# Kernel tuning notes

Hardware: AMD Instinct MI355X
Metric: run time of the kernel (lower is better)

Reference implementation:

```python
import jax, jax.numpy as jnp
import numpy as np

N = 100000
IN = 128
HID = 128
E = 1000000
EP = 100000


def setup_inputs() -> dict:
    key = jax.random.key(0)
    ks = jax.random.split(key, 20)
    inp = {
        "x": jax.random.normal(ks[0], (N, IN), dtype=jnp.float32),
        "edge_src1": jax.random.randint(ks[1], (E,), 0, N),
        "edge_dst1": jax.random.randint(ks[2], (E,), 0, N),
        "edge_src2": jax.random.randint(ks[3], (E,), 0, N),
        "edge_dst2": jax.random.randint(ks[4], (E,), 0, N),
        "pos_src": jax.random.randint(ks[5], (EP,), 0, N),
        "pos_dst": jax.random.randint(ks[6], (EP,), 0, N),
        "neg_src": jax.random.randint(ks[7], (EP,), 0, N),
        "neg_dst": jax.random.randint(ks[8], (EP,), 0, N),
        # SAGEConv layer 1 (in->hid): fc_self (no bias), fc_neigh, shared bias
        "W_self1": jax.random.normal(ks[9], (IN, HID), dtype=jnp.float32) * (1.0 / np.sqrt(IN)),
        "W_neigh1": jax.random.normal(ks[10], (IN, HID), dtype=jnp.float32) * (1.0 / np.sqrt(IN)),
        "b1": jnp.zeros((HID,), dtype=jnp.float32),
        # SAGEConv layer 2 (hid->hid)
        "W_self2": jax.random.normal(ks[11], (HID, HID), dtype=jnp.float32) * (1.0 / np.sqrt(HID)),
        "W_neigh2": jax.random.normal(ks[12], (HID, HID), dtype=jnp.float32) * (1.0 / np.sqrt(HID)),
        "b2": jnp.zeros((HID,), dtype=jnp.float32),
        # predictor: Linear(hid,hid) -> ReLU -> Linear(hid,1)
        "Wp1": jax.random.normal(ks[13], (HID, HID), dtype=jnp.float32) * (1.0 / np.sqrt(HID)),
        "bp1": jnp.zeros((HID,), dtype=jnp.float32),
        "Wp2": jax.random.normal(ks[14], (HID, 1), dtype=jnp.float32) * (1.0 / np.sqrt(HID)),
        "bp2": jnp.zeros((1,), dtype=jnp.float32),
    }
    return inp


def _sage_conv(h, src, dst, W_self, W_neigh, b):
    # mean aggregation over incoming edges: gather h[src], scatter-add to dst, divide by degree
    agg = jax.ops.segment_sum(h[src], dst, num_segments=N)          # [N, d]
    deg = jax.ops.segment_sum(jnp.ones((src.shape[0],), h.dtype), dst, num_segments=N)
    mean = agg / jnp.maximum(deg, 1.0)[:, None]
    return h @ W_self + mean @ W_neigh + b


def _predictor(z, Wp1, bp1, Wp2, bp2):
    return jax.nn.relu(z @ Wp1 + bp1) @ Wp2 + bp2                   # [Ep, 1]


def reference(x, edge_src1, edge_dst1, edge_src2, edge_dst2,
              pos_src, pos_dst, neg_src, neg_dst,
              W_self1, W_neigh1, b1, W_self2, W_neigh2, b2,
              Wp1, bp1, Wp2, bp2):
    h = jax.nn.relu(_sage_conv(x, edge_src1, edge_dst1, W_self1, W_neigh1, b1))
    h = _sage_conv(h, edge_src2, edge_dst2, W_self2, W_neigh2, b2)  # [N, HID]
    h_pos = _predictor(h[pos_src] * h[pos_dst], Wp1, bp1, Wp2, bp2)
    h_neg = _predictor(h[neg_src] * h[neg_dst], Wp1, bp1, Wp2, bp2)
    return (h_pos, h_neg)
```

## Files before the change

kernel.cpp:

```cpp
#include <hip/hip_runtime.h>

typedef unsigned short ushort_t;
typedef __attribute__((ext_vector_type(8))) short short8;
typedef __attribute__((ext_vector_type(4))) float f32x4;

constexpr int NN = 100000;
constexpr int D  = 128;
constexpr int NE = 1000000;
constexpr int NP = 100000;

constexpr int BK_SHIFT = 9;
constexpr int NBK_L = (NN + 511) >> BK_SHIFT;
constexpr int NBK   = 2 * NBK_L;
constexpr int ACHUNK = 4096;
constexpr int ABLOCKS = (2 * NE + ACHUNK - 1) / ACHUNK;

__device__ __forceinline__ float bf2f(ushort_t u) {
    union { unsigned int i; float f; } v; v.i = ((unsigned int)u) << 16; return v.f;
}
__device__ __forceinline__ ushort_t f2bf(float x) {
    union { float f; unsigned int i; } v; v.f = x;
    unsigned int r = v.i + 0x7fffu + ((v.i >> 16) & 1u);
    return (ushort_t)(r >> 16);
}
__device__ __forceinline__ void split2(float x, ushort_t& h, ushort_t& l) {
    h = f2bf(x);
    l = f2bf(x - bf2f(h));
}

__global__ void __launch_bounds__(256) prep_kernel(
    const float* __restrict__ x,
    const float* __restrict__ Ws1, const float* __restrict__ Wn1,
    const float* __restrict__ Ws2, const float* __restrict__ Wn2,
    const float* __restrict__ Wp1,
    ushort_t* __restrict__ xh, ushort_t* __restrict__ xl,
    ushort_t* __restrict__ w1h, ushort_t* __restrict__ w1l,
    ushort_t* __restrict__ w2h, ushort_t* __restrict__ w2l,
    ushort_t* __restrict__ wph, ushort_t* __restrict__ wpl)
{
    int b = blockIdx.x;
    if (b < 12500) {
        int tid = b * 256 + threadIdx.x;
        float4 v = *reinterpret_cast<const float4*>(x + (size_t)tid * 4);
        ushort4 h4, l4;
        split2(v.x, h4.x, l4.x); split2(v.y, h4.y, l4.y);
        split2(v.z, h4.z, l4.z); split2(v.w, h4.w, l4.w);
        *reinterpret_cast<ushort4*>(xh + (size_t)tid * 4) = h4;
        *reinterpret_cast<ushort4*>(xl + (size_t)tid * 4) = l4;
    } else if (b < 12756) {
        int layer2 = (b >= 12628);
        int tid = (b - (layer2 ? 12628 : 12500)) * 256 + threadIdx.x;
        int k = tid >> 7, n = tid & 127;
        const float* Ws = layer2 ? Ws2 : Ws1;
        const float* Wn = layer2 ? Wn2 : Wn1;
        ushort_t* Wth = layer2 ? w2h : w1h;
        ushort_t* Wtl = layer2 ? w2l : w1l;
        float v = (k < 128) ? Ws[k * 128 + n] : Wn[(k - 128) * 128 + n];
        ushort_t h, l; split2(v, h, l);
        Wth[n * 256 + k] = h; Wtl[n * 256 + k] = l;
    } else {
        int tid = (b - 12756) * 256 + threadIdx.x;
        int k = tid >> 7, n = tid & 127;
        float v = Wp1[k * 128 + n];
        ushort_t h, l; split2(v, h, l);
        wph[n * 128 + k] = h; wpl[n * 128 + k] = l;
    }
}

__global__ void __launch_bounds__(256) bucket_count_kernel(
    const int* __restrict__ ed1, const int* __restrict__ ed2,
    int* __restrict__ btot)
{
    __shared__ int hist[NBK];
    int t = threadIdx.x;
    for (int i = t; i < NBK; i += 256) hist[i] = 0;
    __syncthreads();
    int base = blockIdx.x * ACHUNK;
    for (int it = 0; it < ACHUNK / 256; ++it) {
        int e = base + it * 256 + t;
        if (e < 2 * NE) {
            int layer2 = (e >= NE);
            int d = layer2 ? ed2[e - NE] : ed1[e];
            atomicAdd(&hist[(layer2 ? NBK_L : 0) + (d >> BK_SHIFT)], 1);
        }
    }
    __syncthreads();
    for (int i = t; i < NBK; i += 256)
        if (hist[i]) atomicAdd(&btot[i], hist[i]);
}

__global__ void __launch_bounds__(512) bucket_scan_kernel(
    const int* __restrict__ btot, int* __restrict__ bbase, int* __restrict__ bcur)
{
    __shared__ int s[512];
    int t = threadIdx.x;
    int v = (t < NBK) ? btot[t] : 0;
    s[t] = v;
    __syncthreads();
    for (int off = 1; off < 512; off <<= 1) {
        int u = (t >= off) ? s[t - off] : 0;
        __syncthreads();
        s[t] += u;
        __syncthreads();
    }
    if (t < NBK) {
        int ex = s[t] - v;
        bbase[t] = ex;
        bcur[t] = ex;
        if (t == NBK - 1) bbase[NBK] = s[t];
    }
}

__global__ void __launch_bounds__(256) bucket_scatter_kernel(
    const int* __restrict__ es1, const int* __restrict__ ed1,
    const int* __restrict__ es2, const int* __restrict__ ed2,
    int* __restrict__ bcur, int2* __restrict__ pair)
{
    __shared__ int hist[NBK];
    __shared__ int rbase[NBK];
    __shared__ int cur[NBK];
    int t = threadIdx.x;
    for (int i = t; i < NBK; i += 256) hist[i] = 0;
    __syncthreads();
    int base = blockIdx.x * ACHUNK;
    for (int it = 0; it < ACHUNK / 256; ++it) {
        int e = base + it * 256 + t;
        if (e < 2 * NE) {
            int layer2 = (e >= NE);
            int d = layer2 ? ed2[e - NE] : ed1[e];
            atomicAdd(&hist[(layer2 ? NBK_L : 0) + (d >> BK_SHIFT)], 1);
        }
    }
    __syncthreads();
    for (int i = t; i < NBK; i += 256) {
        int h = hist[i];
        rbase[i] = h ? atomicAdd(&bcur[i], h) : 0;
        cur[i] = 0;
    }
    __syncthreads();
    for (int it = 0; it < ACHUNK / 256; ++it) {
        int e = base + it * 256 + t;
        if (e < 2 * NE) {
            int layer2 = (e >= NE);
            int s = layer2 ? es2[e - NE] : es1[e];
            int d = layer2 ? ed2[e - NE] : ed1[e];
            int bkt = (layer2 ? NBK_L : 0) + (d >> BK_SHIFT);
            int r = atomicAdd(&cur[bkt], 1);
            pair[(size_t)rbase[bkt] + r] = make_int2(s, d);
        }
    }
}

__global__ void __launch_bounds__(256) bucket_build_kernel(
    const int2* __restrict__ pair, const int* __restrict__ bbase,
    int* __restrict__ row_off, int* __restrict__ csr)
{
    __shared__ int cnt[512];
    __shared__ int sc[256];
    int b = blockIdx.x;
    int t = threadIdx.x;
    int layer2 = (b >= NBK_L);
    int n0 = (b - (layer2 ? NBK_L : 0)) << BK_SHIFT;
    int nodes = min(512, NN - n0);
    int gnode0 = n0 + (layer2 ? NN : 0);
    int e0 = bbase[b], e1 = bbase[b + 1];
    int m = e1 - e0;

    cnt[t] = 0; cnt[t + 256] = 0;
    __syncthreads();
    for (int j = t; j < m; j += 256)
        atomicAdd(&cnt[pair[(size_t)e0 + j].y - n0], 1);
    __syncthreads();

    int a0 = cnt[2 * t], a1 = cnt[2 * t + 1];
    sc[t] = a0 + a1;
    __syncthreads();
    for (int off = 1; off < 256; off <<= 1) {
        int u = (t >= off) ? sc[t - off] : 0;
        __syncthreads();
        sc[t] += u;
        __syncthreads();
    }
    int ex = sc[t] - (a0 + a1);
    cnt[2 * t] = ex;
    cnt[2 * t + 1] = ex + a0;
    __syncthreads();

    for (int i = t; i < nodes; i += 256)
        row_off[gnode0 + i] = e0 + cnt[i];
    if (b == NBK - 1 && t == 0) row_off[2 * NN] = 2 * NE;
    __syncthreads();

    for (int j = t; j < m; j += 256) {
        int2 p = pair[(size_t)e0 + j];
        int r = atomicAdd(&cnt[p.y - n0], 1);
        csr[(size_t)e0 + r] = p.x;
    }
}

__global__ void __launch_bounds__(256) gather_mean_kernel(
    const float* __restrict__ feat,
    const int* __restrict__ row_off,
    const int* __restrict__ csr,
    ushort_t* __restrict__ mh, ushort_t* __restrict__ ml)
{
    int tid = blockIdx.x * 256 + threadIdx.x;
    int g = tid >> 5;
    int lane = tid & 31;
    int c = lane << 2;
    int beg = row_off[g], end = row_off[g + 1];
    float ax0 = 0.f, ay0 = 0.f, az0 = 0.f, aw0 = 0.f;
    float ax1 = 0.f, ay1 = 0.f, az1 = 0.f, aw1 = 0.f;
    int j = beg;
    for (; j + 8 <= end; j += 8) {
        int s0 = csr[j + 0], s1 = csr[j + 1], s2 = csr[j + 2], s3 = csr[j + 3];
        int s4 = csr[j + 4], s5 = csr[j + 5], s6 = csr[j + 6], s7 = csr[j + 7];
        float4 v0 = *reinterpret_cast<const float4*>(feat + (size_t)s0 * D + c);
        float4 v1 = *reinterpret_cast<const float4*>(feat + (size_t)s1 * D + c);
        float4 v2 = *reinterpret_cast<const float4*>(feat + (size_t)s2 * D + c);
        float4 v3 = *reinterpret_cast<const float4*>(feat + (size_t)s3 * D + c);
        float4 v4 = *reinterpret_cast<const float4*>(feat + (size_t)s4 * D + c);
        float4 v5 = *reinterpret_cast<const float4*>(feat + (size_t)s5 * D + c);
        float4 v6 = *reinterpret_cast<const float4*>(feat + (size_t)s6 * D + c);
        float4 v7 = *reinterpret_cast<const float4*>(feat + (size_t)s7 * D + c);
        ax0 += v0.x + v1.x + v4.x + v5.x; ay0 += v0.y + v1.y + v4.y + v5.y;
        az0 += v0.z + v1.z + v4.z + v5.z; aw0 += v0.w + v1.w + v4.w + v5.w;
        ax1 += v2.x + v3.x + v6.x + v7.x; ay1 += v2.y + v3.y + v6.y + v7.y;
        az1 += v2.z + v3.z + v6.z + v7.z; aw1 += v2.w + v3.w + v6.w + v7.w;
    }
    for (; j < end; ++j) {
        int s = csr[j];
        float4 v = *reinterpret_cast<const float4*>(feat + (size_t)s * D + c);
        ax0 += v.x; ay0 += v.y; az0 += v.z; aw0 += v.w;
    }
    float rd = 1.0f / fmaxf((float)(end - beg), 1.0f);
    float mx = (ax0 + ax1) * rd, my = (ay0 + ay1) * rd;
    float mz = (az0 + az1) * rd, mw = (aw0 + aw1) * rd;
    ushort4 h4, l4;
    split2(mx, h4.x, l4.x); split2(my, h4.y, l4.y);
    split2(mz, h4.z, l4.z); split2(mw, h4.w, l4.w);
    *reinterpret_cast<ushort4*>(mh + (size_t)g * D + c) = h4;
    *reinterpret_cast<ushort4*>(ml + (size_t)g * D + c) = l4;
}

template<bool RELU, bool WSPLIT, bool WF32>
__global__ void __launch_bounds__(512) mfma_sage_gemm(
    const ushort_t* __restrict__ Ah_self, const ushort_t* __restrict__ Al_self,
    const ushort_t* __restrict__ Ah_nei,  const ushort_t* __restrict__ Al_nei,
    const ushort_t* __restrict__ Wth, const ushort_t* __restrict__ Wtl,
    const float* __restrict__ bias,
    ushort_t* __restrict__ out_h, ushort_t* __restrict__ out_l,
    float* __restrict__ out_f)
{
    __shared__ short Bh[128 * 64];
    __shared__ short Bl[128 * 64];

    int t = threadIdx.x;
    int l = t & 63, w = t >> 6;
    int lrow = l & 15, kg = l >> 4;
    int row0 = blockIdx.x * 128;
    int arow = row0 + w * 16 + lrow;
    int arow_c = min(arow, NN - 1);

    f32x4 acc[8];
    for (int i = 0; i < 8; ++i) acc[i] = (f32x4)(0.f);

    for (int half = 0; half < 2; ++half) {
        const ushort_t* Ah = half ? Ah_nei : Ah_self;
        const ushort_t* Al = half ? Al_nei : Al_self;
        for (int kc2 = 0; kc2 < 2; ++kc2) {
            int kcat = half * 128 + kc2 * 64;
            __syncthreads();
            for (int i = 0; i < 2; ++i) {
                int s = t + i * 512;
                int n = s >> 3;
                int k8 = (s & 7) * 8;
                short8 vh = *reinterpret_cast<const short8*>(Wth + n * 256 + kcat + k8);
                short8 vl = *reinterpret_cast<const short8*>(Wtl + n * 256 + kcat + k8);
                int db = n * 128 + ((k8 * 2) ^ ((n & 7) << 4));
                *reinterpret_cast<short8*>((char*)Bh + db) = vh;
                *reinterpret_cast<short8*>((char*)Bl + db) = vl;
            }
            __syncthreads();

            for (int ks = 0; ks < 2; ++ks) {
                int ka = kc2 * 64 + ks * 32 + kg * 8;
                short8 ah = *reinterpret_cast<const short8*>(Ah + (size_t)arow_c * D + ka);
                short8 al = *reinterpret_cast<const short8*>(Al + (size_t)arow_c * D + ka);
                int kb2 = (ks * 32 + kg * 8) * 2;
                for (int ct = 0; ct < 8; ++ct) {
                    int n = ct * 16 + lrow;
                    int db = n * 128 + (kb2 ^ ((n & 7) << 4));
                    short8 bh = *reinterpret_cast<const short8*>((char*)Bh + db);
                    short8 bl = *reinterpret_cast<const short8*>((char*)Bl + db);
                    acc[ct] = __builtin_amdgcn_mfma_f32_16x16x32_bf16(ah, bh, acc[ct], 0, 0, 0);
                    acc[ct] = __builtin_amdgcn_mfma_f32_16x16x32_bf16(ah, bl, acc[ct], 0, 0, 0);
                    acc[ct] = __builtin_amdgcn_mfma_f32_16x16x32_bf16(al, bh, acc[ct], 0, 0, 0);
                }
            }
        }
    }

    for (int ct = 0; ct < 8; ++ct) {
        int n = ct * 16 + lrow;
        float bv = bias[n];
        for (int j = 0; j < 4; ++j) {
            int r = row0 + w * 16 + kg * 4 + j;
            if (r >= NN) continue;
            float y = acc[ct][j] + bv;
            if (RELU) y = fmaxf(y, 0.f);
            if (WF32) out_f[(size_t)r * D + n] = y;
            if (WSPLIT) {
                ushort_t hh, ll; split2(y, hh, ll);
                out_h[(size_t)r * D + n] = hh;
                out_l[(size_t)r * D + n] = ll;
            }
        }
    }
}

__global__ void __launch_bounds__(512) mfma_predictor(
    const float* __restrict__ H,
    const int* __restrict__ ps, const int* __restrict__ pd,
    const int* __restrict__ ns, const int* __restrict__ nd,
    const ushort_t* __restrict__ Wth, const ushort_t* __restrict__ Wtl,
    const float* __restrict__ bp1,
    const float* __restrict__ Wp2, const float* __restrict__ bp2,
    float* __restrict__ out)
{
    __shared__ short Zh[64 * 128];
    __shared__ short Zl[64 * 128];
    __shared__ short Bh[128 * 64];
    __shared__ short Bl[128 * 64];
    __shared__ float red[2][64];

    int t = threadIdx.x;
    int l = t & 63, w = t >> 6;
    int rt = w >> 1, ch = w & 1;
    int lrow = l & 15, kg = l >> 4;
    int row0 = blockIdx.x * 64;

    for (int i = 0; i < 4; ++i) {
        int idx = t + i * 512;
        int r = idx >> 5;
        int c4 = (idx & 31) << 2;
        int p = row0 + r;
        int s  = (p < NP) ? ps[p] : ns[p - NP];
        int d2 = (p < NP) ? pd[p] : nd[p - NP];
        float4 a = *reinterpret_cast<const float4*>(H + (size_t)s * D + c4);
        float4 b = *reinterpret_cast<const float4*>(H + (size_t)d2 * D + c4);
        float z0 = a.x * b.x, z1 = a.y * b.y, z2 = a.z * b.z, z3 = a.w * b.w;
        ushort4 h4, l4;
        split2(z0, h4.x, l4.x); split2(z1, h4.y, l4.y);
        split2(z2, h4.z, l4.z); split2(z3, h4.w, l4.w);
        int db = r * 256 + ((c4 * 2) ^ ((r & 7) << 4));
        *reinterpret_cast<ushort4*>((char*)Zh + db) = h4;
        *reinterpret_cast<ushort4*>((char*)Zl + db) = l4;
    }

    f32x4 acc[4];
    for (int i = 0; i < 4; ++i) acc[i] = (f32x4)(0.f);

    for (int kc = 0; kc < 2; ++kc) {
        __syncthreads();
        for (int i = 0; i < 2; ++i) {
            int s = t + i * 512;
            int n = s >> 3;
            int k8 = (s & 7) * 8;
            short8 vh = *reinterpret_cast<const short8*>(Wth + n * 128 + kc * 64 + k8);
            short8 vl = *reinterpret_cast<const short8*>(Wtl + n * 128 + kc * 64 + k8);
            int db = n * 128 + ((k8 * 2) ^ ((n & 7) << 4));
            *reinterpret_cast<short8*>((char*)Bh + db) = vh;
            *reinterpret_cast<short8*>((char*)Bl + db) = vl;
        }
        __syncthreads();

        for (int ks = 0; ks < 2; ++ks) {
            int zrow = rt * 16 + lrow;
            int kz2 = (kc * 64 + ks * 32 + kg * 8) * 2;
            int za = zrow * 256 + (kz2 ^ ((zrow & 7) << 4));
            short8 ah = *reinterpret_cast<const short8*>((char*)Zh + za);
            short8 al = *reinterpret_cast<const short8*>((char*)Zl + za);
            int kb2 = (ks * 32 + kg * 8) * 2;
            for (int ct = 0; ct < 4; ++ct) {
                int n = ch * 64 + ct * 16 + lrow;
                int db = n * 128 + (kb2 ^ ((n & 7) << 4));
                short8 bh = *reinterpret_cast<const short8*>((char*)Bh + db);
                short8 bl = *reinterpret_cast<const short8*>((char*)Bl + db);
                acc[ct] = __builtin_amdgcn_mfma_f32_16x16x32_bf16(ah, bh, acc[ct], 0, 0, 0);
                acc[ct] = __builtin_amdgcn_mfma_f32_16x16x32_bf16(ah, bl, acc[ct], 0, 0, 0);
                acc[ct] = __builtin_amdgcn_mfma_f32_16x16x32_bf16(al, bh, acc[ct], 0, 0, 0);
            }
        }
    }

    float partial[4] = {0.f, 0.f, 0.f, 0.f};
    for (int ct = 0; ct < 4; ++ct) {
        int n = ch * 64 + ct * 16 + lrow;
        float bv = bp1[n];
        float w2 = Wp2[n];
        for (int j = 0; j < 4; ++j) {
            float y = acc[ct][j] + bv;
            partial[j] += fmaxf(y, 0.f) * w2;
        }
    }
    for (int j = 0; j < 4; ++j)
        for (int off = 8; off >= 1; off >>= 1)
            partial[j] += __shfl_xor(partial[j], off);
    if (lrow == 0)
        for (int j = 0; j < 4; ++j)
            red[ch][rt * 16 + kg * 4 + j] = partial[j];
    __syncthreads();
    if (t < 64)
        out[row0 + t] = red[0][t] + red[1][t] + bp2[0];
}

extern "C" void kernel_launch(void* const* d_in, const int* in_sizes, int n_in,
                              void* d_out, int out_size, void* d_ws, size_t ws_size,
                              hipStream_t stream) {
    const float* x   = (const float*)d_in[0];
    const int*   es1 = (const int*)d_in[1];
    const int*   ed1 = (const int*)d_in[2];
    const int*   es2 = (const int*)d_in[3];
    const int*   ed2 = (const int*)d_in[4];
    const int*   ps  = (const int*)d_in[5];
    const int*   pd  = (const int*)d_in[6];
    const int*   ns  = (const int*)d_in[7];
    const int*   nd  = (const int*)d_in[8];
    const float* Ws1 = (const float*)d_in[9];
    const float* Wn1 = (const float*)d_in[10];
    const float* b1  = (const float*)d_in[11];
    const float* Ws2 = (const float*)d_in[12];
    const float* Wn2 = (const float*)d_in[13];
    const float* b2  = (const float*)d_in[14];
    const float* Wp1 = (const float*)d_in[15];
    const float* bp1 = (const float*)d_in[16];
    const float* Wp2 = (const float*)d_in[17];
    const float* bp2 = (const float*)d_in[18];
    float* out = (float*)d_out;

    char* ws = (char*)d_ws;
    size_t halfb = (size_t)NN * D * sizeof(ushort_t);
    ushort_t* x_h    = (ushort_t*)(ws);
    ushort_t* x_l    = (ushort_t*)(ws + halfb);
    ushort_t* mean_h = (ushort_t*)(ws + 2 * halfb);
    ushort_t* mean_l = (ushort_t*)(ws + 3 * halfb);
    float*    hf     = (float*)(ws + 4 * halfb);
    int2*     pair   = (int2*)hf;
    char* wsp = ws + 4 * halfb + (size_t)NN * D * sizeof(float);
    ushort_t* w1t_h  = (ushort_t*)wsp;
    ushort_t* w1t_l  = w1t_h + 256 * 128;
    ushort_t* w2t_h  = w1t_l + 256 * 128;
    ushort_t* w2t_l  = w2t_h + 256 * 128;
    ushort_t* wpt_h  = w2t_l + 256 * 128;
    ushort_t* wpt_l  = wpt_h + 128 * 128;
    int* row_off = (int*)(wpt_l + 128 * 128 + 64);
    int* csr     = row_off + 2 * NN + 2;
    int* btot    = csr + 2 * NE;
    int* bbase   = btot + NBK;
    int* bcur    = bbase + NBK + 1;

    dim3 blk(256), blk512(512);
    int gatherBlocks = NN * 32 / 256;
    int gemmBlocks   = (NN + 127) / 128;
    int predBlocks   = 2 * NP / 64;

    hipMemsetAsync(btot, 0, NBK * sizeof(int), stream);
    prep_kernel<<<12820, blk, 0, stream>>>(
        x, Ws1, Wn1, Ws2, Wn2, Wp1,
        x_h, x_l, w1t_h, w1t_l, w2t_h, w2t_l, wpt_h, wpt_l);
    bucket_count_kernel<<<ABLOCKS, blk, 0, stream>>>(ed1, ed2, btot);
    bucket_scan_kernel<<<1, 512, 0, stream>>>(btot, bbase, bcur);
    bucket_scatter_kernel<<<ABLOCKS, blk, 0, stream>>>(es1, ed1, es2, ed2, bcur, pair);
    bucket_build_kernel<<<NBK, blk, 0, stream>>>(pair, bbase, row_off, csr);

    gather_mean_kernel<<<gatherBlocks, blk, 0, stream>>>(x, row_off, csr, mean_h, mean_l);
    mfma_sage_gemm<true, true, true><<<gemmBlocks, blk512, 0, stream>>>(
        x_h, x_l, mean_h, mean_l, w1t_h, w1t_l, b1, x_h, x_l, hf);

    gather_mean_kernel<<<gatherBlocks, blk, 0, stream>>>(hf, row_off + NN, csr, mean_h, mean_l);
    mfma_sage_gemm<false, false, true><<<gemmBlocks, blk512, 0, stream>>>(
        x_h, x_l, mean_h, mean_l, w2t_h, w2t_l, b2, nullptr, nullptr, hf);

    mfma_predictor<<<predBlocks, blk512, 0, stream>>>(
        hf, ps, pd, ns, nd, wpt_h, wpt_l, bp1, Wp2, bp2, out);
}
```

Baseline: 366.4 us.

## Fuse neighbor mean gather into SAGE GEMM with LDS-staged split-bf16 tiles

```diff
diff --git a/kernel.cpp b/kernel.cpp
--- a/kernel.cpp
+++ b/kernel.cpp
@@ -15,6 +15,10 @@
 constexpr int ACHUNK = 4096;
 constexpr int ABLOCKS = (2 * NE + ACHUNK - 1) / ACHUNK;
 
+constexpr int PB_W   = 256;
+constexpr int PB_WP  = PB_W + 64;
+constexpr int PB_CNT = PB_WP + ABLOCKS;
+
 __device__ __forceinline__ float bf2f(ushort_t u) {
     union { unsigned int i; float f; } v; v.i = ((unsigned int)u) << 16; return v.f;
 }
@@ -29,27 +33,21 @@
 }
 
 __global__ void __launch_bounds__(256) prep_kernel(
-    const float* __restrict__ x,
     const float* __restrict__ Ws1, const float* __restrict__ Wn1,
     const float* __restrict__ Ws2, const float* __restrict__ Wn2,
     const float* __restrict__ Wp1,
-    ushort_t* __restrict__ xh, ushort_t* __restrict__ xl,
+    const int* __restrict__ ed1, const int* __restrict__ ed2,
     ushort_t* __restrict__ w1h, ushort_t* __restrict__ w1l,
     ushort_t* __restrict__ w2h, ushort_t* __restrict__ w2l,
-    ushort_t* __restrict__ wph, ushort_t* __restrict__ wpl)
-{
+    ushort_t* __restrict__ wph, ushort_t* __restrict__ wpl,
+    int* __restrict__ btot)
+{
+    __shared__ int hist[NBK];
     int b = blockIdx.x;
-    if (b < 12500) {
-        int tid = b * 256 + threadIdx.x;
-        float4 v = *reinterpret_cast<const float4*>(x + (size_t)tid * 4);
-        ushort4 h4, l4;
-        split2(v.x, h4.x, l4.x); split2(v.y, h4.y, l4.y);
-        split2(v.z, h4.z, l4.z); split2(v.w, h4.w, l4.w);
-        *reinterpret_cast<ushort4*>(xh + (size_t)tid * 4) = h4;
-        *reinterpret_cast<ushort4*>(xl + (size_t)tid * 4) = l4;
-    } else if (b < 12756) {
-        int layer2 = (b >= 12628);
-        int tid = (b - (layer2 ? 12628 : 12500)) * 256 + threadIdx.x;
+    int t = threadIdx.x;
+    if (b < PB_W) {
+        int layer2 = (b >= 128);
+        int tid = (b - (layer2 ? 128 : 0)) * 256 + t;
         int k = tid >> 7, n = tid & 127;
         const float* Ws = layer2 ? Ws2 : Ws1;
         const float* Wn = layer2 ? Wn2 : Wn1;
@@ -58,35 +56,28 @@
         float v = (k < 128) ? Ws[k * 128 + n] : Wn[(k - 128) * 128 + n];
         ushort_t h, l; split2(v, h, l);
         Wth[n * 256 + k] = h; Wtl[n * 256 + k] = l;
-    } else {
-        int tid = (b - 12756) * 256 + threadIdx.x;
+    } else if (b < PB_WP) {
+        int tid = (b - PB_W) * 256 + t;
         int k = tid >> 7, n = tid & 127;
         float v = Wp1[k * 128 + n];
         ushort_t h, l; split2(v, h, l);
         wph[n * 128 + k] = h; wpl[n * 128 + k] = l;
-    }
-}
-
-__global__ void __launch_bounds__(256) bucket_count_kernel(
-    const int* __restrict__ ed1, const int* __restrict__ ed2,
-    int* __restrict__ btot)
-{
-    __shared__ int hist[NBK];
-    int t = threadIdx.x;
-    for (int i = t; i < NBK; i += 256) hist[i] = 0;
-    __syncthreads();
-    int base = blockIdx.x * ACHUNK;
-    for (int it = 0; it < ACHUNK / 256; ++it) {
-        int e = base + it * 256 + t;
-        if (e < 2 * NE) {
-            int layer2 = (e >= NE);
-            int d = layer2 ? ed2[e - NE] : ed1[e];
-            atomicAdd(&hist[(layer2 ? NBK_L : 0) + (d >> BK_SHIFT)], 1);
-        }
-    }
-    __syncthreads();
-    for (int i = t; i < NBK; i += 256)
-        if (hist[i]) atomicAdd(&btot[i], hist[i]);
+    } else {
+        for (int i = t; i < NBK; i += 256) hist[i] = 0;
+        __syncthreads();
+        int base = (b - PB_WP) * ACHUNK;
+        for (int it = 0; it < ACHUNK / 256; ++it) {
+            int e = base + it * 256 + t;
+            if (e < 2 * NE) {
+                int layer2 = (e >= NE);
+                int d = layer2 ? ed2[e - NE] : ed1[e];
+                atomicAdd(&hist[(layer2 ? NBK_L : 0) + (d >> BK_SHIFT)], 1);
+            }
+        }
+        __syncthreads();
+        for (int i = t; i < NBK; i += 256)
+            if (hist[i]) atomicAdd(&btot[i], hist[i]);
+    }
 }
 
 __global__ void __launch_bounds__(512) bucket_scan_kernel(
@@ -198,81 +189,77 @@
     }
 }
 
-__global__ void __launch_bounds__(256) gather_mean_kernel(
+template<bool RELU>
+__global__ void __launch_bounds__(256) fused_conv_kernel(
     const float* __restrict__ feat,
     const int* __restrict__ row_off,
     const int* __restrict__ csr,
-    ushort_t* __restrict__ mh, ushort_t* __restrict__ ml)
-{
-    int tid = blockIdx.x * 256 + threadIdx.x;
-    int g = tid >> 5;
-    int lane = tid & 31;
-    int c = lane << 2;
-    int beg = row_off[g], end = row_off[g + 1];
-    float ax0 = 0.f, ay0 = 0.f, az0 = 0.f, aw0 = 0.f;
-    float ax1 = 0.f, ay1 = 0.f, az1 = 0.f, aw1 = 0.f;
-    int j = beg;
-    for (; j + 8 <= end; j += 8) {
-        int s0 = csr[j + 0], s1 = csr[j + 1], s2 = csr[j + 2], s3 = csr[j + 3];
-        int s4 = csr[j + 4], s5 = csr[j + 5], s6 = csr[j + 6], s7 = csr[j + 7];
-        float4 v0 = *reinterpret_cast<const float4*>(feat + (size_t)s0 * D + c);
-        float4 v1 = *reinterpret_cast<const float4*>(feat + (size_t)s1 * D + c);
-        float4 v2 = *reinterpret_cast<const float4*>(feat + (size_t)s2 * D + c);
-        float4 v3 = *reinterpret_cast<const float4*>(feat + (size_t)s3 * D + c);
-        float4 v4 = *reinterpret_cast<const float4*>(feat + (size_t)s4 * D + c);
-        float4 v5 = *reinterpret_cast<const float4*>(feat + (size_t)s5 * D + c);
-        float4 v6 = *reinterpret_cast<const float4*>(feat + (size_t)s6 * D + c);
-        float4 v7 = *reinterpret_cast<const float4*>(feat + (size_t)s7 * D + c);
-        ax0 += v0.x + v1.x + v4.x + v5.x; ay0 += v0.y + v1.y + v4.y + v5.y;
-        az0 += v0.z + v1.z + v4.z + v5.z; aw0 += v0.w + v1.w + v4.w + v5.w;
-        ax1 += v2.x + v3.x + v6.x + v7.x; ay1 += v2.y + v3.y + v6.y + v7.y;
-        az1 += v2.z + v3.z + v6.z + v7.z; aw1 += v2.w + v3.w + v6.w + v7.w;
-    }
-    for (; j < end; ++j) {
-        int s = csr[j];
-        float4 v = *reinterpret_cast<const float4*>(feat + (size_t)s * D + c);
-        ax0 += v.x; ay0 += v.y; az0 += v.z; aw0 += v.w;
-    }
-    float rd = 1.0f / fmaxf((float)(end - beg), 1.0f);
-    float mx = (ax0 + ax1) * rd, my = (ay0 + ay1) * rd;
-    float mz = (az0 + az1) * rd, mw = (aw0 + aw1) * rd;
-    ushort4 h4, l4;
-    split2(mx, h4.x, l4.x); split2(my, h4.y, l4.y);
-    split2(mz, h4.z, l4.z); split2(mw, h4.w, l4.w);
-    *reinterpret_cast<ushort4*>(mh + (size_t)g * D + c) = h4;
-    *reinterpret_cast<ushort4*>(ml + (size_t)g * D + c) = l4;
-}
-
-template<bool RELU, bool WSPLIT, bool WF32>
-__global__ void __launch_bounds__(512) mfma_sage_gemm(
-    const ushort_t* __restrict__ Ah_self, const ushort_t* __restrict__ Al_self,
-    const ushort_t* __restrict__ Ah_nei,  const ushort_t* __restrict__ Al_nei,
     const ushort_t* __restrict__ Wth, const ushort_t* __restrict__ Wtl,
     const float* __restrict__ bias,
-    ushort_t* __restrict__ out_h, ushort_t* __restrict__ out_l,
-    float* __restrict__ out_f)
-{
+    float* __restrict__ out)
+{
+    __shared__ short Mh[64 * 128];
+    __shared__ short Ml[64 * 128];
     __shared__ short Bh[128 * 64];
     __shared__ short Bl[128 * 64];
 
     int t = threadIdx.x;
+    int row0 = blockIdx.x * 64;
+
+    {
+        int gi = t >> 5, lane = t & 31, c = lane << 2;
+        for (int rr = gi; rr < 64; rr += 8) {
+            int node = min(row0 + rr, NN - 1);
+            int j = row_off[node], e = row_off[node + 1];
+            int deg = e - j;
+            float ax0 = 0.f, ay0 = 0.f, az0 = 0.f, aw0 = 0.f;
+            float ax1 = 0.f, ay1 = 0.f, az1 = 0.f, aw1 = 0.f;
+            for (; j + 8 <= e; j += 8) {
+                int s0 = csr[j], s1 = csr[j+1], s2 = csr[j+2], s3 = csr[j+3];
+                int s4 = csr[j+4], s5 = csr[j+5], s6 = csr[j+6], s7 = csr[j+7];
+                float4 v0 = *reinterpret_cast<const float4*>(feat + (size_t)s0 * D + c);
+                float4 v1 = *reinterpret_cast<const float4*>(feat + (size_t)s1 * D + c);
+                float4 v2 = *reinterpret_cast<const float4*>(feat + (size_t)s2 * D + c);
+                float4 v3 = *reinterpret_cast<const float4*>(feat + (size_t)s3 * D + c);
+                float4 v4 = *reinterpret_cast<const float4*>(feat + (size_t)s4 * D + c);
+                float4 v5 = *reinterpret_cast<const float4*>(feat + (size_t)s5 * D + c);
+                float4 v6 = *reinterpret_cast<const float4*>(feat + (size_t)s6 * D + c);
+                float4 v7 = *reinterpret_cast<const float4*>(feat + (size_t)s7 * D + c);
+                ax0 += v0.x + v1.x + v4.x + v5.x; ay0 += v0.y + v1.y + v4.y + v5.y;
+                az0 += v0.z + v1.z + v4.z + v5.z; aw0 += v0.w + v1.w + v4.w + v5.w;
+                ax1 += v2.x + v3.x + v6.x + v7.x; ay1 += v2.y + v3.y + v6.y + v7.y;
+                az1 += v2.z + v3.z + v6.z + v7.z; aw1 += v2.w + v3.w + v6.w + v7.w;
+            }
+            for (; j < e; ++j) {
+                int s = csr[j];
+                float4 v = *reinterpret_cast<const float4*>(feat + (size_t)s * D + c);
+                ax0 += v.x; ay0 += v.y; az0 += v.z; aw0 += v.w;
+            }
+            float rd = 1.0f / fmaxf((float)deg, 1.0f);
+            float mx = (ax0 + ax1) * rd, my = (ay0 + ay1) * rd;
+            float mz = (az0 + az1) * rd, mw = (aw0 + aw1) * rd;
+            ushort4 h4, l4;
+            split2(mx, h4.x, l4.x); split2(my, h4.y, l4.y);
+            split2(mz, h4.z, l4.z); split2(mw, h4.w, l4.w);
+            int db = rr * 256 + ((c * 2) ^ ((rr & 7) << 4));
+            *reinterpret_cast<ushort4*>((char*)Mh + db) = h4;
+            *reinterpret_cast<ushort4*>((char*)Ml + db) = l4;
+        }
+    }
+
     int l = t & 63, w = t >> 6;
     int lrow = l & 15, kg = l >> 4;
-    int row0 = blockIdx.x * 128;
-    int arow = row0 + w * 16 + lrow;
-    int arow_c = min(arow, NN - 1);
+    int arow_c = min(row0 + w * 16 + lrow, NN - 1);
 
     f32x4 acc[8];
     for (int i = 0; i < 8; ++i) acc[i] = (f32x4)(0.f);
 
     for (int half = 0; half < 2; ++half) {
-        const ushort_t* Ah = half ? Ah_nei : Ah_self;
-        const ushort_t* Al = half ? Al_nei : Al_self;
         for (int kc2 = 0; kc2 < 2; ++kc2) {
             int kcat = half * 128 + kc2 * 64;
             __syncthreads();
-            for (int i = 0; i < 2; ++i) {
-                int s = t + i * 512;
+            for (int i = 0; i < 4; ++i) {
+                int s = t + i * 256;
                 int n = s >> 3;
                 int k8 = (s & 7) * 8;
                 short8 vh = *reinterpret_cast<const short8*>(Wth + n * 256 + kcat + k8);
@@ -285,8 +272,26 @@
 
             for (int ks = 0; ks < 2; ++ks) {
                 int ka = kc2 * 64 + ks * 32 + kg * 8;
-                short8 ah = *reinterpret_cast<const short8*>(Ah + (size_t)arow_c * D + ka);
-                short8 al = *reinterpret_cast<const short8*>(Al + (size_t)arow_c * D + ka);
+                short8 ah, al;
+                if (half == 0) {
+                    const float* p = feat + (size_t)arow_c * D + ka;
+                    float4 v0 = *reinterpret_cast<const float4*>(p);
+                    float4 v1 = *reinterpret_cast<const float4*>(p + 4);
+                    ushort_t hh, ll;
+                    split2(v0.x, hh, ll); ah[0] = hh; al[0] = ll;
+                    split2(v0.y, hh, ll); ah[1] = hh; al[1] = ll;
+                    split2(v0.z, hh, ll); ah[2] = hh; al[2] = ll;
+                    split2(v0.w, hh, ll); ah[3] = hh; al[3] = ll;
+                    split2(v1.x, hh, ll); ah[4] = hh; al[4] = ll;
+                    split2(v1.y, hh, ll); ah[5] = hh; al[5] = ll;
+                    split2(v1.z, hh, ll); ah[6] = hh; al[6] = ll;
+                    split2(v1.w, hh, ll); ah[7] = hh; al[7] = ll;
+                } else {
+                    int row = w * 16 + lrow;
+                    int db = row * 256 + ((ka * 2) ^ ((row & 7) << 4));
+                    ah = *reinterpret_cast<const short8*>((char*)Mh + db);
+                    al = *reinterpret_cast<const short8*>((char*)Ml + db);
+                }
                 int kb2 = (ks * 32 + kg * 8) * 2;
                 for (int ct = 0; ct < 8; ++ct) {
                     int n = ct * 16 + lrow;
@@ -309,12 +314,7 @@
             if (r >= NN) continue;
             float y = acc[ct][j] + bv;
             if (RELU) y = fmaxf(y, 0.f);
-            if (WF32) out_f[(size_t)r * D + n] = y;
-            if (WSPLIT) {
-                ushort_t hh, ll; split2(y, hh, ll);
-                out_h[(size_t)r * D + n] = hh;
-                out_l[(size_t)r * D + n] = ll;
-            }
+            out[(size_t)r * D + n] = y;
         }
     }
 }
@@ -440,14 +440,11 @@
     float* out = (float*)d_out;
 
     char* ws = (char*)d_ws;
-    size_t halfb = (size_t)NN * D * sizeof(ushort_t);
-    ushort_t* x_h    = (ushort_t*)(ws);
-    ushort_t* x_l    = (ushort_t*)(ws + halfb);
-    ushort_t* mean_h = (ushort_t*)(ws + 2 * halfb);
-    ushort_t* mean_l = (ushort_t*)(ws + 3 * halfb);
-    float*    hf     = (float*)(ws + 4 * halfb);
-    int2*     pair   = (int2*)hf;
-    char* wsp = ws + 4 * halfb + (size_t)NN * D * sizeof(float);
+    size_t fb = (size_t)NN * D * sizeof(float);
+    float* h  = (float*)(ws);
+    float* h2 = (float*)(ws + fb);
+    int2*  pair = (int2*)h2;
+    char* wsp = ws + 2 * fb;
     ushort_t* w1t_h  = (ushort_t*)wsp;
     ushort_t* w1t_l  = w1t_h + 256 * 128;
     ushort_t* w2t_h  = w1t_l + 256 * 128;
@@ -461,27 +458,23 @@
     int* bcur    = bbase + NBK + 1;
 
     dim3 blk(256), blk512(512);
-    int gatherBlocks = NN * 32 / 256;
-    int gemmBlocks   = (NN + 127) / 128;
-    int predBlocks   = 2 * NP / 64;
+    int convBlocks = (NN + 63) / 64;
+    int predBlocks = 2 * NP / 64;
 
     hipMemsetAsync(btot, 0, NBK * sizeof(int), stream);
-    prep_kernel<<<12820, blk, 0, stream>>>(
-        x, Ws1, Wn1, Ws2, Wn2, Wp1,
-        x_h, x_l, w1t_h, w1t_l, w2t_h, w2t_l, wpt_h, wpt_l);
-    bucket_count_kernel<<<ABLOCKS, blk, 0, stream>>>(ed1, ed2, btot);
+    prep_kernel<<<PB_CNT, blk, 0, stream>>>(
+        Ws1, Wn1, Ws2, Wn2, Wp1, ed1, ed2,
+        w1t_h, w1t_l, w2t_h, w2t_l, wpt_h, wpt_l, btot);
     bucket_scan_kernel<<<1, 512, 0, stream>>>(btot, bbase, bcur);
     bucket_scatter_kernel<<<ABLOCKS, blk, 0, stream>>>(es1, ed1, es2, ed2, bcur, pair);
     bucket_build_kernel<<<NBK, blk, 0, stream>>>(pair, bbase, row_off, csr);
 
-    gather_mean_kernel<<<gatherBlocks, blk, 0, stream>>>(x, row_off, csr, mean_h, mean_l);
-    mfma_sage_gemm<true, true, true><<<gemmBlocks, blk512, 0, stream>>>(
-        x_h, x_l, mean_h, mean_l, w1t_h, w1t_l, b1, x_h, x_l, hf);
-
-    gather_mean_kernel<<<gatherBlocks, blk, 0, stream>>>(hf, row_off + NN, csr, mean_h, mean_l);
-    mfma_sage_gemm<false, false, true><<<gemmBlocks, blk512, 0, stream>>>(
-        x_h, x_l, mean_h, mean_l, w2t_h, w2t_l, b2, nullptr, nullptr, hf);
+    fused_conv_kernel<true><<<convBlocks, blk, 0, stream>>>(
+        x, row_off, csr, w1t_h, w1t_l, b1, h);
+
+    fused_conv_kernel<false><<<convBlocks, blk, 0, stream>>>(
+        h, row_off + NN, csr, w2t_h, w2t_l, b2, h2);
 
     mfma_predictor<<<predBlocks, blk512, 0, stream>>>(
-        hf, ps, pd, ns, nd, wpt_h, wpt_l, bp1, Wp2, bp2, out);
-}
+        h2, ps, pd, ns, nd, wpt_h, wpt_l, bp1, Wp2, bp2, out);
+}
```

New measurement: 465.1 us. +27.0%, slower.
